# Optimization experiments

Measured on AMD Instinct MI355X. Metric: run time of the kernel, lower is better.

Reference implementation:

```python
import jax, jax.numpy as jnp
import numpy as np

B, S, D, H = 2, 2048, 1024, 16
HD = D // H  # head_dim = 64
EPS = 1e-12


def setup_inputs() -> dict:
    key = jax.random.key(0)
    ks = jax.random.split(key, 12)
    s = 0.02
    return {
        "hidden_states": jax.random.normal(ks[0], (B, S, D), jnp.float32),
        "attention_mask": jnp.zeros((B, 1, 1, S), jnp.float32),
        "alibi_bias": jax.random.normal(ks[1], (1, H, S, S), jnp.float32) * 0.1,
        "Wq": jax.random.normal(ks[2], (D, D), jnp.float32) * s,
        "bq": jnp.zeros((D,), jnp.float32),
        "Wk": jax.random.normal(ks[3], (D, D), jnp.float32) * s,
        "bk": jnp.zeros((D,), jnp.float32),
        "Wv": jax.random.normal(ks[4], (D, D), jnp.float32) * s,
        "bv": jnp.zeros((D,), jnp.float32),
        "Wo": jax.random.normal(ks[5], (D, D), jnp.float32) * s,
        "bo": jnp.zeros((D,), jnp.float32),
        "ln_gamma": jnp.ones((D,), jnp.float32),
        "ln_beta": jnp.zeros((D,), jnp.float32),
    }


def _split_heads(x):
    # [B, S, D] -> [B, H, S, HD]
    return x.reshape(B, S, H, HD).transpose(0, 2, 1, 3)


def reference(hidden_states, attention_mask, alibi_bias,
              Wq, bq, Wk, bk, Wv, bv, Wo, bo, ln_gamma, ln_beta):
    q = _split_heads(hidden_states @ Wq + bq)
    k = _split_heads(hidden_states @ Wk + bk)
    v = _split_heads(hidden_states @ Wv + bv)

    scale = HD ** -0.5
    # combined additive mask: [B,1,1,S] + [1,H,S,S] -> broadcast [B,H,S,S]
    combined_mask = attention_mask + alibi_bias
    scores = jnp.einsum('bhqd,bhkd->bhqk', q, k) * scale + combined_mask
    probs = jax.nn.softmax(scores, axis=-1)
    attn = jnp.einsum('bhqk,bhkd->bhqd', probs, v)  # [B,H,S,HD]
    attn = attn.transpose(0, 2, 1, 3).reshape(B, S, D)

    out = attn @ Wo + bo
    x = hidden_states + out  # post-norm residual
    mu = jnp.mean(x, axis=-1, keepdims=True)
    var = jnp.mean(jnp.square(x - mu), axis=-1, keepdims=True)
    return (x - mu) * jax.lax.rsqrt(var + EPS) * ln_gamma + ln_beta
```

## Files before the change

### kernel.cpp

```cpp
#include <hip/hip_runtime.h>

#define Bb 2
#define Ss 2048
#define Dd 1024
#define Hh 16
#define HD 64
#define Mm (Bb*Ss)

typedef __bf16 bf16;
typedef __bf16 bf16x8 __attribute__((ext_vector_type(8)));
typedef float f32x4 __attribute__((ext_vector_type(4)));

__device__ __forceinline__ void gload_lds16(const bf16* g, bf16* l) {
    __builtin_amdgcn_global_load_lds(
        (const __attribute__((address_space(1))) unsigned int*)g,
        (__attribute__((address_space(3))) unsigned int*)l,
        16, 0, 0);
}

__global__ void cvt_f32_bf16(const float* __restrict__ in, bf16* __restrict__ out, int n4) {
    int i = blockIdx.x * blockDim.x + threadIdx.x;
    if (i < n4) {
        float4 v = *(const float4*)(in + i * 4);
        out[i*4+0] = (bf16)v.x; out[i*4+1] = (bf16)v.y;
        out[i*4+2] = (bf16)v.z; out[i*4+3] = (bf16)v.w;
    }
}

__global__ void wtrans(const float* __restrict__ W0, const float* __restrict__ W1,
                       const float* __restrict__ W2, const float* __restrict__ W3,
                       bf16* __restrict__ O0, bf16* __restrict__ O1,
                       bf16* __restrict__ O2, bf16* __restrict__ O3) {
    const float* W = (blockIdx.z == 0) ? W0 : (blockIdx.z == 1) ? W1 : (blockIdx.z == 2) ? W2 : W3;
    bf16* O = (blockIdx.z == 0) ? O0 : (blockIdx.z == 1) ? O1 : (blockIdx.z == 2) ? O2 : O3;
    __shared__ bf16 t[64][65];
    int k0 = blockIdx.x * 64, n0 = blockIdx.y * 64;
    for (int c = threadIdx.x; c < 4096; c += 256) {
        int r = c >> 6, cc = c & 63;
        t[r][cc] = (bf16)W[(k0 + r) * Dd + n0 + cc];
    }
    __syncthreads();
    for (int c = threadIdx.x; c < 4096; c += 256) {
        int r = c >> 6, cc = c & 63;
        O[(n0 + r) * Dd + k0 + cc] = t[cc][r];
    }
}

__global__ __launch_bounds__(256, 3)
void gemm_bt(const bf16* __restrict__ A, const bf16* __restrict__ Bt,
             const float* __restrict__ b0, const float* __restrict__ b1, const float* __restrict__ b2,
             bf16* __restrict__ o0, bf16* __restrict__ o1, bf16* __restrict__ o2, int mode) {
    const int K = 1024;
    __shared__ __align__(16) bf16 As[128 * 32];
    __shared__ __align__(16) bf16 Bs[128 * 32];
    int tid = threadIdx.x;
    int wave = tid >> 6, lane = tid & 63;
    int lane15 = lane & 15, quad = lane >> 4;
    int wm = (wave >> 1) * 64, wn = (wave & 1) * 64;
    int m0 = blockIdx.x * 128, n0 = blockIdx.y * 128;
    int lrow = lane >> 2, lcol = (lane & 3) * 8;
    const bf16* Ag = &A[(size_t)(m0 + wave * 16 + lrow) * K + lcol];
    const bf16* Bg = &Bt[(size_t)(n0 + wave * 16 + lrow) * K + lcol];
    bf16* Asw = &As[wave * 16 * 32];
    bf16* Bsw = &Bs[wave * 16 * 32];

    f32x4 acc[4][4] = {};

    for (int kt = 0; kt < K; kt += 32) {
        __syncthreads();
        gload_lds16(Ag + kt,           Asw);
        gload_lds16(Ag + 64 * K + kt,  Asw + 64 * 32);
        gload_lds16(Bg + kt,           Bsw);
        gload_lds16(Bg + 64 * K + kt,  Bsw + 64 * 32);
        __syncthreads();
        bf16x8 af[4], bfr[4];
#pragma unroll
        for (int i = 0; i < 4; i++) af[i] = *(const bf16x8*)(&As[(wm + i * 16 + lane15) * 32 + quad * 8]);
#pragma unroll
        for (int j = 0; j < 4; j++) bfr[j] = *(const bf16x8*)(&Bs[(wn + j * 16 + lane15) * 32 + quad * 8]);
#pragma unroll
        for (int i = 0; i < 4; i++)
#pragma unroll
            for (int j = 0; j < 4; j++)
                acc[i][j] = __builtin_amdgcn_mfma_f32_16x16x32_bf16(af[i], bfr[j], acc[i][j], 0, 0, 0);
    }

#pragma unroll
    for (int i = 0; i < 4; i++) {
        int mbase = m0 + wm + i * 16 + quad * 4;
#pragma unroll
        for (int j = 0; j < 4; j++) {
            int n = n0 + wn + j * 16 + lane15;
            if (mode == 0) {
                float bv = b0[n];
#pragma unroll
                for (int r = 0; r < 4; r++)
                    o0[(size_t)(mbase + r) * 1024 + n] = (bf16)(acc[i][j][r] + bv);
            } else {
                int which = n >> 10, nn = n & 1023;
                const float* bp = (which == 0) ? b0 : (which == 1) ? b1 : b2;
                bf16* op = (which == 0) ? o0 : (which == 1) ? o1 : o2;
                float bv = bp[nn];
                int hh = nn >> 6, hd = nn & 63;
#pragma unroll
                for (int r = 0; r < 4; r++) {
                    int m = mbase + r;
                    int bb = m >> 11, s = m & 2047;
                    op[(((size_t)(bb * Hh + hh) * Ss + s) * HD) + hd] = (bf16)(acc[i][j][r] + bv);
                }
            }
        }
    }
}

__global__ __launch_bounds__(256, 4)
void attn_kernel(const bf16* __restrict__ Q, const bf16* __restrict__ Kk, const bf16* __restrict__ V,
                 const float* __restrict__ alibi, const float* __restrict__ mask,
                 bf16* __restrict__ outattn) {
    int qt = blockIdx.x, h = blockIdx.y, b = blockIdx.z;
    __shared__ __align__(16) bf16 Ks[64 * 64];
    __shared__ __align__(16) bf16 Vts[64 * 64];
    __shared__ __align__(16) bf16 QPs[64 * 64];
    __shared__ __align__(16) float Als[64 * 64];
    int tid = threadIdx.x, wave = tid >> 6, lane = tid & 63;
    int lane15 = lane & 15, quad = lane >> 4;

    const bf16* Qbase = Q + ((size_t)(b * Hh + h) * Ss + qt * 64) * HD;
    const bf16* Kbase = Kk + (size_t)(b * Hh + h) * Ss * HD;
    const bf16* Vbase = V + (size_t)(b * Hh + h) * Ss * HD;
    const float* Abase = alibi + ((size_t)h * Ss + qt * 64) * Ss;
    const float* mask_base = mask + (size_t)b * Ss;

    for (int c = tid; c < 512; c += 256) {
        int r = c >> 3, off = (c & 7) * 8;
        *(bf16x8*)(&QPs[r * 64 + (off ^ ((r & 7) * 8))]) = *(const bf16x8*)(&Qbase[r * HD + off]);
    }
    __syncthreads();
    int qrow = wave * 16 + lane15;
    bf16x8 qf0 = *(const bf16x8*)(&QPs[qrow * 64 + ((quad * 8) ^ ((qrow & 7) * 8))]);
    bf16x8 qf1 = *(const bf16x8*)(&QPs[qrow * 64 + ((32 + quad * 8) ^ ((qrow & 7) * 8))]);

    float m_i[4], l_i[4];
    f32x4 O[4] = {};
#pragma unroll
    for (int r = 0; r < 4; r++) { m_i[r] = -1e30f; l_i[r] = 0.f; }

    const float scale = 0.125f;

    for (int kt = 0; kt < Ss; kt += 64) {
        __syncthreads();
        for (int c = tid; c < 512; c += 256) {
            int r = c >> 3, off = (c & 7) * 8;
            *(bf16x8*)(&Ks[r * 64 + (off ^ ((r & 7) * 8))]) = *(const bf16x8*)(&Kbase[(size_t)(kt + r) * HD + off]);
        }
        for (int c = tid; c < 512; c += 256) {
            int r = c >> 3, off = (c & 7) * 8;
            bf16x8 v = *(const bf16x8*)(&Vbase[(size_t)(kt + r) * HD + off]);
#pragma unroll
            for (int e = 0; e < 8; e++) {
                int d = off + e;
                Vts[d * 64 + (r ^ ((((d & 7) ^ ((d >> 3) & 7))) * 8))] = v[e];
            }
        }
        for (int c = tid; c < 1024; c += 256) {
            int r = c >> 4, c4 = (c & 15) * 4;
            *(float4*)(&Als[r * 64 + (c4 ^ (((r >> 2) & 1) * 16 + ((r >> 3) & 1) * 8))]) =
                *(const float4*)(&Abase[(size_t)r * Ss + kt + c4]);
        }
        __syncthreads();

        f32x4 sc[4];
        f32x4 z = {0.f, 0.f, 0.f, 0.f};
#pragma unroll
        for (int j = 0; j < 4; j++) {
            int krow = j * 16 + lane15;
            bf16x8 kf0 = *(const bf16x8*)(&Ks[krow * 64 + ((quad * 8) ^ ((krow & 7) * 8))]);
            bf16x8 kf1 = *(const bf16x8*)(&Ks[krow * 64 + ((32 + quad * 8) ^ ((krow & 7) * 8))]);
            f32x4 s = __builtin_amdgcn_mfma_f32_16x16x32_bf16(qf0, kf0, z, 0, 0, 0);
            s = __builtin_amdgcn_mfma_f32_16x16x32_bf16(qf1, kf1, s, 0, 0, 0);
            sc[j] = s;
        }
#pragma unroll
        for (int j = 0; j < 4; j++) {
            int col = j * 16 + lane15;
            float mk = mask_base[kt + col];
#pragma unroll
            for (int r = 0; r < 4; r++) {
                int row = wave * 16 + quad * 4 + r;
                float al = Als[row * 64 + (col ^ (((row >> 2) & 1) * 16 + ((row >> 3) & 1) * 8))];
                sc[j][r] = sc[j][r] * scale + al + mk;
            }
        }
        float alpha[4];
#pragma unroll
        for (int r = 0; r < 4; r++) {
            float v = fmaxf(fmaxf(sc[0][r], sc[1][r]), fmaxf(sc[2][r], sc[3][r]));
#pragma unroll
            for (int d = 1; d < 16; d <<= 1) v = fmaxf(v, __shfl_xor(v, d, 64));
            float mnew = fmaxf(m_i[r], v);
            alpha[r] = __expf(m_i[r] - mnew);
            m_i[r] = mnew;
        }
        float rs[4] = {0.f, 0.f, 0.f, 0.f};
#pragma unroll
        for (int j = 0; j < 4; j++)
#pragma unroll
            for (int r = 0; r < 4; r++) {
                float p = __expf(sc[j][r] - m_i[r]);
                sc[j][r] = p;
                rs[r] += p;
            }
#pragma unroll
        for (int r = 0; r < 4; r++) {
            float v = rs[r];
#pragma unroll
            for (int d = 1; d < 16; d <<= 1) v += __shfl_xor(v, d, 64);
            l_i[r] = l_i[r] * alpha[r] + v;
        }
#pragma unroll
        for (int j = 0; j < 4; j++)
#pragma unroll
            for (int r = 0; r < 4; r++) {
                int row = wave * 16 + quad * 4 + r;
                QPs[row * 64 + ((j * 16 + lane15) ^ ((row & 7) * 8))] = (bf16)sc[j][r];
            }
        __syncthreads();

        int prow = wave * 16 + lane15;
        bf16x8 pf0 = *(const bf16x8*)(&QPs[prow * 64 + ((quad * 8) ^ ((prow & 7) * 8))]);
        bf16x8 pf1 = *(const bf16x8*)(&QPs[prow * 64 + ((32 + quad * 8) ^ ((prow & 7) * 8))]);
#pragma unroll
        for (int jd = 0; jd < 4; jd++) {
            int vrow = jd * 16 + lane15;
            int vs = (((vrow & 7) ^ ((vrow >> 3) & 7)) * 8);
#pragma unroll
            for (int r = 0; r < 4; r++) O[jd][r] *= alpha[r];
            bf16x8 vf0 = *(const bf16x8*)(&Vts[vrow * 64 + ((quad * 8) ^ vs)]);
            bf16x8 vf1 = *(const bf16x8*)(&Vts[vrow * 64 + ((32 + quad * 8) ^ vs)]);
            O[jd] = __builtin_amdgcn_mfma_f32_16x16x32_bf16(pf0, vf0, O[jd], 0, 0, 0);
            O[jd] = __builtin_amdgcn_mfma_f32_16x16x32_bf16(pf1, vf1, O[jd], 0, 0, 0);
        }
    }

#pragma unroll
    for (int jd = 0; jd < 4; jd++) {
        int d = jd * 16 + lane15;
#pragma unroll
        for (int r = 0; r < 4; r++) {
            int qg = qt * 64 + wave * 16 + quad * 4 + r;
            float v = O[jd][r] / l_i[r];
            outattn[(((size_t)b * Ss + qg) * Hh + h) * HD + d] = (bf16)v;
        }
    }
}

__global__ void ln_kernel(const float* __restrict__ hidden, const bf16* __restrict__ Y,
                          const float* __restrict__ gamma, const float* __restrict__ beta,
                          float* __restrict__ out) {
    int row = blockIdx.x;
    int tid = threadIdx.x, wave = tid >> 6, lane = tid & 63;
    float x[4];
    float s = 0.f, q = 0.f;
#pragma unroll
    for (int e = 0; e < 4; e++) {
        int col = e * 256 + tid;
        x[e] = hidden[(size_t)row * Dd + col] + (float)Y[(size_t)row * Dd + col];
        s += x[e];
        q += x[e] * x[e];
    }
#pragma unroll
    for (int d = 1; d < 64; d <<= 1) { s += __shfl_xor(s, d, 64); q += __shfl_xor(q, d, 64); }
    __shared__ float sm[4], sq[4];
    if (lane == 0) { sm[wave] = s; sq[wave] = q; }
    __syncthreads();
    float tot = sm[0] + sm[1] + sm[2] + sm[3];
    float totq = sq[0] + sq[1] + sq[2] + sq[3];
    float mu = tot * (1.f / 1024.f);
    float var = totq * (1.f / 1024.f) - mu * mu;
    float rstd = rsqrtf(var + 1e-12f);
#pragma unroll
    for (int e = 0; e < 4; e++) {
        int col = e * 256 + tid;
        out[(size_t)row * Dd + col] = (x[e] - mu) * rstd * gamma[col] + beta[col];
    }
}

extern "C" void kernel_launch(void* const* d_in, const int* in_sizes, int n_in,
                              void* d_out, int out_size, void* d_ws, size_t ws_size,
                              hipStream_t stream) {
    const float* hidden = (const float*)d_in[0];
    const float* amask  = (const float*)d_in[1];
    const float* alibi  = (const float*)d_in[2];
    const float* Wq = (const float*)d_in[3];
    const float* bq = (const float*)d_in[4];
    const float* Wk = (const float*)d_in[5];
    const float* bk = (const float*)d_in[6];
    const float* Wv = (const float*)d_in[7];
    const float* bv = (const float*)d_in[8];
    const float* Wo = (const float*)d_in[9];
    const float* bo = (const float*)d_in[10];
    const float* ln_g = (const float*)d_in[11];
    const float* ln_b = (const float*)d_in[12];
    float* out = (float*)d_out;

    char* w = (char*)d_ws;
    bf16* Xb   = (bf16*)(w);
    bf16* WqT  = (bf16*)(w + 8388608);
    bf16* WkT  = (bf16*)(w + 10485760);
    bf16* WvT  = (bf16*)(w + 12582912);
    bf16* WoT  = (bf16*)(w + 14680064);
    bf16* Qw   = (bf16*)(w + 16777216);
    bf16* Kw   = (bf16*)(w + 25165824);
    bf16* Vw   = (bf16*)(w + 33554432);
    bf16* Attn = (bf16*)(w + 41943040);
    bf16* Yw   = (bf16*)(w + 50331648);

    cvt_f32_bf16<<<4096, 256, 0, stream>>>(hidden, Xb, Mm * Dd / 4);
    wtrans<<<dim3(16, 16, 4), 256, 0, stream>>>(Wq, Wk, Wv, Wo, WqT, WkT, WvT, WoT);

    gemm_bt<<<dim3(32, 24), 256, 0, stream>>>(Xb, WqT, bq, bk, bv, Qw, Kw, Vw, 1);

    attn_kernel<<<dim3(32, 16, 2), 256, 0, stream>>>(Qw, Kw, Vw, alibi, amask, Attn);

    gemm_bt<<<dim3(32, 8), 256, 0, stream>>>(Attn, WoT, bo, nullptr, nullptr, Yw, nullptr, nullptr, 0);

    ln_kernel<<<4096, 256, 0, stream>>>(hidden, Yw, ln_g, ln_b, out);
}
```

Measured before the change: 637.1 us.

## Double-buffer GEMM tiles, prefetch K/V in registers, stream alibi directly

```diff
diff --git a/kernel.cpp b/kernel.cpp
--- a/kernel.cpp
+++ b/kernel.cpp
@@ -46,47 +46,57 @@
     }
 }
 
-__global__ __launch_bounds__(256, 3)
+template<int BM>
+__global__ __launch_bounds__(256, (BM == 64) ? 4 : 3)
 void gemm_bt(const bf16* __restrict__ A, const bf16* __restrict__ Bt,
              const float* __restrict__ b0, const float* __restrict__ b1, const float* __restrict__ b2,
              bf16* __restrict__ o0, bf16* __restrict__ o1, bf16* __restrict__ o2, int mode) {
     const int K = 1024;
-    __shared__ __align__(16) bf16 As[128 * 32];
-    __shared__ __align__(16) bf16 Bs[128 * 32];
+    constexpr int MI = BM / 32;
+    __shared__ __align__(16) bf16 As[2][BM * 32];
+    __shared__ __align__(16) bf16 Bs[2][128 * 32];
     int tid = threadIdx.x;
     int wave = tid >> 6, lane = tid & 63;
     int lane15 = lane & 15, quad = lane >> 4;
-    int wm = (wave >> 1) * 64, wn = (wave & 1) * 64;
-    int m0 = blockIdx.x * 128, n0 = blockIdx.y * 128;
+    int wm = (wave >> 1) * (BM / 2), wn = (wave & 1) * 64;
+    int m0 = blockIdx.x * BM, n0 = blockIdx.y * 128;
     int lrow = lane >> 2, lcol = (lane & 3) * 8;
     const bf16* Ag = &A[(size_t)(m0 + wave * 16 + lrow) * K + lcol];
     const bf16* Bg = &Bt[(size_t)(n0 + wave * 16 + lrow) * K + lcol];
-    bf16* Asw = &As[wave * 16 * 32];
-    bf16* Bsw = &Bs[wave * 16 * 32];
-
-    f32x4 acc[4][4] = {};
-
+
+    f32x4 acc[MI][4] = {};
+
+#define STAGE(buf, kt) do { \
+        bf16* Asw = &As[buf][wave * 16 * 32]; \
+        bf16* Bsw = &Bs[buf][wave * 16 * 32]; \
+        gload_lds16(Ag + (kt), Asw); \
+        if constexpr (BM == 128) gload_lds16(Ag + 64 * K + (kt), Asw + 64 * 32); \
+        gload_lds16(Bg + (kt), Bsw); \
+        gload_lds16(Bg + 64 * K + (kt), Bsw + 64 * 32); \
+    } while (0)
+
+    STAGE(0, 0);
+    __syncthreads();
+    int cur = 0;
     for (int kt = 0; kt < K; kt += 32) {
-        __syncthreads();
-        gload_lds16(Ag + kt,           Asw);
-        gload_lds16(Ag + 64 * K + kt,  Asw + 64 * 32);
-        gload_lds16(Bg + kt,           Bsw);
-        gload_lds16(Bg + 64 * K + kt,  Bsw + 64 * 32);
-        __syncthreads();
-        bf16x8 af[4], bfr[4];
-#pragma unroll
-        for (int i = 0; i < 4; i++) af[i] = *(const bf16x8*)(&As[(wm + i * 16 + lane15) * 32 + quad * 8]);
-#pragma unroll
-        for (int j = 0; j < 4; j++) bfr[j] = *(const bf16x8*)(&Bs[(wn + j * 16 + lane15) * 32 + quad * 8]);
-#pragma unroll
-        for (int i = 0; i < 4; i++)
+        if (kt + 32 < K) STAGE(cur ^ 1, kt + 32);
+        bf16x8 af[MI], bfr[4];
+#pragma unroll
+        for (int i = 0; i < MI; i++) af[i] = *(const bf16x8*)(&As[cur][(wm + i * 16 + lane15) * 32 + quad * 8]);
+#pragma unroll
+        for (int j = 0; j < 4; j++) bfr[j] = *(const bf16x8*)(&Bs[cur][(wn + j * 16 + lane15) * 32 + quad * 8]);
+#pragma unroll
+        for (int i = 0; i < MI; i++)
 #pragma unroll
             for (int j = 0; j < 4; j++)
                 acc[i][j] = __builtin_amdgcn_mfma_f32_16x16x32_bf16(af[i], bfr[j], acc[i][j], 0, 0, 0);
-    }
-
-#pragma unroll
-    for (int i = 0; i < 4; i++) {
+        __syncthreads();
+        cur ^= 1;
+    }
+#undef STAGE
+
+#pragma unroll
+    for (int i = 0; i < MI; i++) {
         int mbase = m0 + wm + i * 16 + quad * 4;
 #pragma unroll
         for (int j = 0; j < 4; j++) {
@@ -121,21 +131,38 @@
     __shared__ __align__(16) bf16 Ks[64 * 64];
     __shared__ __align__(16) bf16 Vts[64 * 64];
     __shared__ __align__(16) bf16 QPs[64 * 64];
-    __shared__ __align__(16) float Als[64 * 64];
     int tid = threadIdx.x, wave = tid >> 6, lane = tid & 63;
     int lane15 = lane & 15, quad = lane >> 4;
 
     const bf16* Qbase = Q + ((size_t)(b * Hh + h) * Ss + qt * 64) * HD;
     const bf16* Kbase = Kk + (size_t)(b * Hh + h) * Ss * HD;
     const bf16* Vbase = V + (size_t)(b * Hh + h) * Ss * HD;
-    const float* Abase = alibi + ((size_t)h * Ss + qt * 64) * Ss;
+    const float* alibi_q = alibi + ((size_t)h * Ss + qt * 64 + wave * 16 + quad * 4) * Ss;
     const float* mask_base = mask + (size_t)b * Ss;
+
+    int sr = tid >> 3, soff = (tid & 7) * 8;
 
     for (int c = tid; c < 512; c += 256) {
         int r = c >> 3, off = (c & 7) * 8;
         *(bf16x8*)(&QPs[r * 64 + (off ^ ((r & 7) * 8))]) = *(const bf16x8*)(&Qbase[r * HD + off]);
     }
+    {
+        bf16x8 k0 = *(const bf16x8*)(&Kbase[(size_t)sr * HD + soff]);
+        bf16x8 k1 = *(const bf16x8*)(&Kbase[(size_t)(sr + 32) * HD + soff]);
+        bf16x8 v0 = *(const bf16x8*)(&Vbase[(size_t)sr * HD + soff]);
+        bf16x8 v1 = *(const bf16x8*)(&Vbase[(size_t)(sr + 32) * HD + soff]);
+        *(bf16x8*)(&Ks[sr * 64 + (soff ^ ((sr & 7) * 8))]) = k0;
+        *(bf16x8*)(&Ks[(sr + 32) * 64 + (soff ^ (((sr + 32) & 7) * 8))]) = k1;
+#pragma unroll
+        for (int e = 0; e < 8; e++) {
+            int d = soff + e;
+            int vs = (((d & 7) ^ ((d >> 3) & 7)) * 8);
+            Vts[d * 64 + (sr ^ vs)] = v0[e];
+            Vts[d * 64 + ((sr + 32) ^ vs)] = v1[e];
+        }
+    }
     __syncthreads();
+
     int qrow = wave * 16 + lane15;
     bf16x8 qf0 = *(const bf16x8*)(&QPs[qrow * 64 + ((quad * 8) ^ ((qrow & 7) * 8))]);
     bf16x8 qf1 = *(const bf16x8*)(&QPs[qrow * 64 + ((32 + quad * 8) ^ ((qrow & 7) * 8))]);
@@ -148,26 +175,24 @@
     const float scale = 0.125f;
 
     for (int kt = 0; kt < Ss; kt += 64) {
-        __syncthreads();
-        for (int c = tid; c < 512; c += 256) {
-            int r = c >> 3, off = (c & 7) * 8;
-            *(bf16x8*)(&Ks[r * 64 + (off ^ ((r & 7) * 8))]) = *(const bf16x8*)(&Kbase[(size_t)(kt + r) * HD + off]);
-        }
-        for (int c = tid; c < 512; c += 256) {
-            int r = c >> 3, off = (c & 7) * 8;
-            bf16x8 v = *(const bf16x8*)(&Vbase[(size_t)(kt + r) * HD + off]);
-#pragma unroll
-            for (int e = 0; e < 8; e++) {
-                int d = off + e;
-                Vts[d * 64 + (r ^ ((((d & 7) ^ ((d >> 3) & 7))) * 8))] = v[e];
-            }
-        }
-        for (int c = tid; c < 1024; c += 256) {
-            int r = c >> 4, c4 = (c & 15) * 4;
-            *(float4*)(&Als[r * 64 + (c4 ^ (((r >> 2) & 1) * 16 + ((r >> 3) & 1) * 8))]) =
-                *(const float4*)(&Abase[(size_t)r * Ss + kt + c4]);
-        }
-        __syncthreads();
+        bool hn = (kt + 64) < Ss;
+        float al[4][4], mk[4];
+#pragma unroll
+        for (int j = 0; j < 4; j++) {
+#pragma unroll
+            for (int r = 0; r < 4; r++)
+                al[j][r] = alibi_q[(size_t)r * Ss + kt + j * 16 + lane15];
+            mk[j] = mask_base[kt + j * 16 + lane15];
+        }
+        bf16x8 kn0, kn1, vn0, vn1;
+        if (hn) {
+            const bf16* Kn = Kbase + (size_t)(kt + 64) * HD;
+            const bf16* Vn = Vbase + (size_t)(kt + 64) * HD;
+            kn0 = *(const bf16x8*)(&Kn[(size_t)sr * HD + soff]);
+            kn1 = *(const bf16x8*)(&Kn[(size_t)(sr + 32) * HD + soff]);
+            vn0 = *(const bf16x8*)(&Vn[(size_t)sr * HD + soff]);
+            vn1 = *(const bf16x8*)(&Vn[(size_t)(sr + 32) * HD + soff]);
+        }
 
         f32x4 sc[4];
         f32x4 z = {0.f, 0.f, 0.f, 0.f};
@@ -181,16 +206,10 @@
             sc[j] = s;
         }
 #pragma unroll
-        for (int j = 0; j < 4; j++) {
-            int col = j * 16 + lane15;
-            float mk = mask_base[kt + col];
-#pragma unroll
-            for (int r = 0; r < 4; r++) {
-                int row = wave * 16 + quad * 4 + r;
-                float al = Als[row * 64 + (col ^ (((row >> 2) & 1) * 16 + ((row >> 3) & 1) * 8))];
-                sc[j][r] = sc[j][r] * scale + al + mk;
-            }
-        }
+        for (int j = 0; j < 4; j++)
+#pragma unroll
+            for (int r = 0; r < 4; r++)
+                sc[j][r] = sc[j][r] * scale + al[j][r] + mk[j];
         float alpha[4];
 #pragma unroll
         for (int r = 0; r < 4; r++) {
@@ -224,8 +243,7 @@
                 int row = wave * 16 + quad * 4 + r;
                 QPs[row * 64 + ((j * 16 + lane15) ^ ((row & 7) * 8))] = (bf16)sc[j][r];
             }
-        __syncthreads();
-
+        asm volatile("s_waitcnt lgkmcnt(0)" ::: "memory");
         int prow = wave * 16 + lane15;
         bf16x8 pf0 = *(const bf16x8*)(&QPs[prow * 64 + ((quad * 8) ^ ((prow & 7) * 8))]);
         bf16x8 pf1 = *(const bf16x8*)(&QPs[prow * 64 + ((32 + quad * 8) ^ ((prow & 7) * 8))]);
@@ -240,6 +258,19 @@
             O[jd] = __builtin_amdgcn_mfma_f32_16x16x32_bf16(pf0, vf0, O[jd], 0, 0, 0);
             O[jd] = __builtin_amdgcn_mfma_f32_16x16x32_bf16(pf1, vf1, O[jd], 0, 0, 0);
         }
+        __syncthreads();
+        if (hn) {
+            *(bf16x8*)(&Ks[sr * 64 + (soff ^ ((sr & 7) * 8))]) = kn0;
+            *(bf16x8*)(&Ks[(sr + 32) * 64 + (soff ^ (((sr + 32) & 7) * 8))]) = kn1;
+#pragma unroll
+            for (int e = 0; e < 8; e++) {
+                int d = soff + e;
+                int vs = (((d & 7) ^ ((d >> 3) & 7)) * 8);
+                Vts[d * 64 + (sr ^ vs)] = vn0[e];
+                Vts[d * 64 + ((sr + 32) ^ vs)] = vn1[e];
+            }
+        }
+        __syncthreads();
     }
 
 #pragma unroll
@@ -318,11 +349,11 @@
     cvt_f32_bf16<<<4096, 256, 0, stream>>>(hidden, Xb, Mm * Dd / 4);
     wtrans<<<dim3(16, 16, 4), 256, 0, stream>>>(Wq, Wk, Wv, Wo, WqT, WkT, WvT, WoT);
 
-    gemm_bt<<<dim3(32, 24), 256, 0, stream>>>(Xb, WqT, bq, bk, bv, Qw, Kw, Vw, 1);
+    gemm_bt<128><<<dim3(32, 24), 256, 0, stream>>>(Xb, WqT, bq, bk, bv, Qw, Kw, Vw, 1);
 
     attn_kernel<<<dim3(32, 16, 2), 256, 0, stream>>>(Qw, Kw, Vw, alibi, amask, Attn);
 
-    gemm_bt<<<dim3(32, 8), 256, 0, stream>>>(Attn, WoT, bo, nullptr, nullptr, Yw, nullptr, nullptr, 0);
+    gemm_bt<64><<<dim3(64, 8), 256, 0, stream>>>(Attn, WoT, bo, nullptr, nullptr, Yw, nullptr, nullptr, 0);
 
     ln_kernel<<<4096, 256, 0, stream>>>(hidden, Yw, ln_g, ln_b, out);
 }
```

Result: slower. 733.8 us (+15.2%).
